# Optimization experiments

Hardware: AMD Instinct MI355X
Metric: run time of the kernel (lower is better)

The kernel has to match this reference:

```python
import jax, jax.numpy as jnp
import numpy as np

N, IN, H, C = 50000, 128, 4, 32
E = 800000
NEG_SLOPE = 0.2


def setup_inputs() -> dict:
    key = jax.random.key(0)
    ks = jax.random.split(key, 8)
    x = jax.random.normal(ks[0], (N, IN), dtype=jnp.float32)
    edge_index = jax.random.randint(ks[1], (2, E), 0, N, dtype=jnp.int64)
    s = 0.1
    W = jax.random.normal(ks[2], (H * C, IN), dtype=jnp.float32) * s
    att_src = jax.random.normal(ks[3], (1, H, C), dtype=jnp.float32) * s
    att_dst = jax.random.normal(ks[4], (1, H, C), dtype=jnp.float32) * s
    bias = jnp.zeros((H * C,), dtype=jnp.float32)
    skip_W = jax.random.normal(ks[5], (H * C, IN), dtype=jnp.float32) * s
    skip_b = jnp.zeros((H * C,), dtype=jnp.float32)
    return {"x": x, "edge_index": edge_index, "W": W, "att_src": att_src,
            "att_dst": att_dst, "bias": bias, "skip_W": skip_W, "skip_b": skip_b}


def reference(x, edge_index, W, att_src, att_dst, bias, skip_W, skip_b):
    src, dst = edge_index[0], edge_index[1]
    # projected node features: [N, H, C]
    xp = (x @ W.T).reshape(N, H, C)
    # per-node attention logits: [N, H]
    a_src = jnp.sum(xp * att_src, axis=-1)
    a_dst = jnp.sum(xp * att_dst, axis=-1)
    # edge logits with LeakyReLU: [E, H]
    e = a_src[src] + a_dst[dst]
    e = jnp.where(e > 0, e, NEG_SLOPE * e)
    # segment softmax over incoming edges of each dst node
    m = jax.ops.segment_max(e, dst, num_segments=N)  # [N, H]
    ex = jnp.exp(e - m[dst])
    denom = jax.ops.segment_sum(ex, dst, num_segments=N)  # [N, H]
    alpha = ex / (denom[dst] + 1e-16)
    # weighted messages and scatter-add aggregation: [N, H, C]
    msg = alpha[:, :, None] * xp[src]
    agg = jax.ops.segment_sum(msg, dst, num_segments=N)
    x_gat = agg.reshape(N, H * C) + bias
    x_skip = x @ skip_W.T + skip_b
    return jax.nn.elu(x_gat + x_skip)
```

## Files before the change

### kernel.cpp

```cpp
#include <hip/hip_runtime.h>
#include <hip/hip_bf16.h>


#define NN 50000
#define EE 800000
#define FD 128
#define NEG_SLOPE 0.2f

#define SCB 1024
#define NB_SC ((NN + SCB - 1) / SCB)
#define NB_HIST (EE / 256)
#define NB_CONVW 32
#define NB_MFMA (NN / 16)

typedef __attribute__((ext_vector_type(8))) short short8;
typedef __attribute__((ext_vector_type(4))) float f32x4;

__device__ inline ushort f2b(float f) {
    __hip_bfloat16 h = __float2bfloat16(f);
    return *reinterpret_cast<ushort*>(&h);
}
__device__ inline float b2f(ushort u) {
    union { float f; unsigned int i; } c;
    c.i = ((unsigned int)u) << 16;
    return c.f;
}

__global__ __launch_bounds__(256) void gat_pre_kernel(
    const int* __restrict__ idx, int* __restrict__ count, int* __restrict__ rank,
    const float* __restrict__ W, const float* __restrict__ skip_W,
    ushort* __restrict__ wb)
{
    int b = blockIdx.x;
    if (b < NB_HIST) {
        int k = b * 256 + threadIdx.x;
        int d = idx[EE + k];
        rank[k] = atomicAdd(&count[d], 1);
    } else {
        int i = ((b - NB_HIST) * 256 + threadIdx.x) * 4;
        int row = i >> 7;
        int colb = i & 127;
        const float* src = (row < 128) ? (W + row * FD + colb)
                                       : (skip_W + (row - 128) * FD + colb);
        float4 v = *reinterpret_cast<const float4*>(src);
        ushort4 o;
        o.x = f2b(v.x); o.y = f2b(v.y); o.z = f2b(v.z); o.w = f2b(v.w);
        *reinterpret_cast<ushort4*>(wb + i) = o;
    }
}

__global__ __launch_bounds__(1024) void gat_blocksum_kernel(
    const int* __restrict__ count, int* __restrict__ bsum)
{
    __shared__ int ws[16];
    int tid = threadIdx.x, lane = tid & 63, wv = tid >> 6;
    int i = blockIdx.x * SCB + tid;
    int v = (i < NN) ? count[i] : 0;
    #pragma unroll
    for (int off = 32; off; off >>= 1) v += __shfl_down(v, off, 64);
    if (lane == 0) ws[wv] = v;
    __syncthreads();
    if (wv == 0) {
        int t = (lane < 16) ? ws[lane] : 0;
        #pragma unroll
        for (int off = 8; off; off >>= 1) t += __shfl_down(t, off, 64);
        if (lane == 0) bsum[blockIdx.x] = t;
    }
}

__global__ __launch_bounds__(1024) void gat_scan_kernel(
    const int* __restrict__ count, const int* __restrict__ bsum,
    int* __restrict__ rowptr)
{
    __shared__ int ws[16];
    __shared__ int boff_s;
    int tid = threadIdx.x, lane = tid & 63, wv = tid >> 6;
    int i = blockIdx.x * SCB + tid;
    int v = (i < NN) ? count[i] : 0;
    int incl = v;
    #pragma unroll
    for (int off = 1; off < 64; off <<= 1) {
        int t = __shfl_up(incl, off, 64);
        if (lane >= off) incl += t;
    }
    if (lane == 63) ws[wv] = incl;
    __syncthreads();
    if (wv == 0) {
        int t = (lane < 16) ? ws[lane] : 0;
        int winc = t;
        #pragma unroll
        for (int off = 1; off < 16; off <<= 1) {
            int u = __shfl_up(winc, off, 64);
            if (lane >= off) winc += u;
        }
        if (lane < 16) ws[lane] = winc - t;
    } else if (wv == 1) {
        int t = (lane < blockIdx.x) ? bsum[lane] : 0;
        #pragma unroll
        for (int off = 32; off; off >>= 1) t += __shfl_down(t, off, 64);
        if (lane == 0) boff_s = t;
    }
    __syncthreads();
    int excl = boff_s + ws[wv] + incl - v;
    if (i < NN) rowptr[i] = excl;
    if (blockIdx.x == 0 && tid == 0) rowptr[NN] = EE;
}

__global__ __launch_bounds__(256) void gat_mfma_fill_kernel(
    const float* __restrict__ x, const ushort* __restrict__ wb,
    const float* __restrict__ att_src, const float* __restrict__ att_dst,
    const float* __restrict__ bias, const float* __restrict__ skip_b,
    ushort* __restrict__ xpb, float* __restrict__ a_src, float* __restrict__ a_dst,
    float* __restrict__ skip,
    const int* __restrict__ idx, const int* __restrict__ rank,
    const int* __restrict__ rowptr, int* __restrict__ col)
{
    if (blockIdx.x >= NB_MFMA) {
        int k = (blockIdx.x - NB_MFMA) * 256 + threadIdx.x;
        int d = idx[EE + k];
        col[rowptr[d] + rank[k]] = idx[k];
        return;
    }

    const int tid = threadIdx.x;
    const int w = tid >> 6;
    const int l = tid & 63;
    const int lrow = l & 15;
    const int lgrp = l >> 4;
    const int m0 = blockIdx.x * 16;
    const int is_skip = w >> 1;
    const int ncb = (w & 1) * 64;

    short8 bfrag[4][4];
    const ushort* wbase = wb + (size_t)(is_skip * 128 + ncb) * FD;
    #pragma unroll
    for (int t = 0; t < 4; ++t)
        #pragma unroll
        for (int kk = 0; kk < 4; ++kk)
            bfrag[t][kk] = *reinterpret_cast<const short8*>(
                wbase + (size_t)(t * 16 + lrow) * FD + kk * 32 + lgrp * 8);

    short8 afrag[4];
    const float* xrow = x + (size_t)(m0 + lrow) * FD + lgrp * 8;
    #pragma unroll
    for (int kk = 0; kk < 4; ++kk) {
        float4 a0 = *reinterpret_cast<const float4*>(xrow + kk * 32);
        float4 a1 = *reinterpret_cast<const float4*>(xrow + kk * 32 + 4);
        short8 af;
        af[0] = f2b(a0.x); af[1] = f2b(a0.y); af[2] = f2b(a0.z); af[3] = f2b(a0.w);
        af[4] = f2b(a1.x); af[5] = f2b(a1.y); af[6] = f2b(a1.z); af[7] = f2b(a1.w);
        afrag[kk] = af;
    }

    f32x4 acc[4];
    #pragma unroll
    for (int t = 0; t < 4; ++t) acc[t] = (f32x4){0.f, 0.f, 0.f, 0.f};

    #pragma unroll
    for (int kk = 0; kk < 4; ++kk)
        #pragma unroll
        for (int t = 0; t < 4; ++t)
            acc[t] = __builtin_amdgcn_mfma_f32_16x16x32_bf16(
                afrag[kk], bfrag[t][kk], acc[t], 0, 0, 0);

    if (is_skip) {
        #pragma unroll
        for (int t = 0; t < 4; ++t) {
            int colt = ncb + t * 16 + lrow;
            float add = skip_b[colt] + bias[colt];
            #pragma unroll
            for (int r = 0; r < 4; ++r) {
                int row = m0 + lgrp * 4 + r;
                skip[(size_t)row * FD + colt] = acc[t][r] + add;
            }
        }
    } else {
        float as[4], ad[4];
        #pragma unroll
        for (int t = 0; t < 4; ++t) {
            int colt = ncb + t * 16 + lrow;
            as[t] = att_src[colt];
            ad[t] = att_dst[colt];
            #pragma unroll
            for (int r = 0; r < 4; ++r) {
                int row = m0 + lgrp * 4 + r;
                xpb[(size_t)row * FD + colt] = f2b(acc[t][r]);
            }
        }
        const int h0 = ncb >> 5;
        #pragma unroll
        for (int r = 0; r < 4; ++r) {
            float p0 = acc[0][r] * as[0] + acc[1][r] * as[1];
            float p1 = acc[2][r] * as[2] + acc[3][r] * as[3];
            float q0 = acc[0][r] * ad[0] + acc[1][r] * ad[1];
            float q1 = acc[2][r] * ad[2] + acc[3][r] * ad[3];
            #pragma unroll
            for (int m = 1; m < 16; m <<= 1) {
                p0 += __shfl_xor(p0, m, 64);
                p1 += __shfl_xor(p1, m, 64);
                q0 += __shfl_xor(q0, m, 64);
                q1 += __shfl_xor(q1, m, 64);
            }
            if (lrow == 0) {
                int row = m0 + lgrp * 4 + r;
                a_src[(size_t)row * 4 + h0]     = p0;
                a_src[(size_t)row * 4 + h0 + 1] = p1;
                a_dst[(size_t)row * 4 + h0]     = q0;
                a_dst[(size_t)row * 4 + h0 + 1] = q1;
            }
        }
    }
}

__global__ __launch_bounds__(256) void gat_gather_kernel(
    const int* __restrict__ rowptr, const int* __restrict__ col,
    const float* __restrict__ a_src, const float* __restrict__ a_dst,
    const ushort* __restrict__ xpb, const float* __restrict__ skip,
    float* __restrict__ out)
{
    int wid = (blockIdx.x * 256 + threadIdx.x) >> 6;
    const int d = __builtin_amdgcn_readfirstlane(wid);
    int lane = threadIdx.x & 63;
    const int h = lane >> 4;
    const int ch = lane * 2;
    const float ad = a_dst[(size_t)d * 4 + h];
    const int beg = rowptr[d], end = rowptr[d + 1];
    float2 sk = *reinterpret_cast<const float2*>(skip + (size_t)d * FD + ch);

    float accx = 0.f, accy = 0.f, asum = 0.f;
    int j = beg;
    for (; j + 4 <= end; j += 4) {
        int s0 = col[j], s1 = col[j + 1], s2 = col[j + 2], s3 = col[j + 3];
        float e0 = a_src[(size_t)s0 * 4 + h] + ad;
        float e1 = a_src[(size_t)s1 * 4 + h] + ad;
        float e2 = a_src[(size_t)s2 * 4 + h] + ad;
        float e3 = a_src[(size_t)s3 * 4 + h] + ad;
        ushort2 x0 = *reinterpret_cast<const ushort2*>(xpb + (size_t)s0 * FD + ch);
        ushort2 x1 = *reinterpret_cast<const ushort2*>(xpb + (size_t)s1 * FD + ch);
        ushort2 x2 = *reinterpret_cast<const ushort2*>(xpb + (size_t)s2 * FD + ch);
        ushort2 x3 = *reinterpret_cast<const ushort2*>(xpb + (size_t)s3 * FD + ch);
        e0 = e0 > 0.f ? e0 : NEG_SLOPE * e0;
        e1 = e1 > 0.f ? e1 : NEG_SLOPE * e1;
        e2 = e2 > 0.f ? e2 : NEG_SLOPE * e2;
        e3 = e3 > 0.f ? e3 : NEG_SLOPE * e3;
        float p0 = __expf(e0), p1 = __expf(e1), p2 = __expf(e2), p3 = __expf(e3);
        asum += (p0 + p1) + (p2 + p3);
        accx += p0 * b2f(x0.x) + p1 * b2f(x1.x) + p2 * b2f(x2.x) + p3 * b2f(x3.x);
        accy += p0 * b2f(x0.y) + p1 * b2f(x1.y) + p2 * b2f(x2.y) + p3 * b2f(x3.y);
    }
    for (; j < end; ++j) {
        int s = col[j];
        float e = a_src[(size_t)s * 4 + h] + ad;
        ushort2 xv = *reinterpret_cast<const ushort2*>(xpb + (size_t)s * FD + ch);
        e = e > 0.f ? e : NEG_SLOPE * e;
        float p = __expf(e);
        asum += p;
        accx += p * b2f(xv.x);
        accy += p * b2f(xv.y);
    }
    float inv = 1.f / (asum + 1e-16f);
    float r0 = sk.x + accx * inv;
    float r1 = sk.y + accy * inv;
    r0 = r0 > 0.f ? r0 : expm1f(r0);
    r1 = r1 > 0.f ? r1 : expm1f(r1);
    *reinterpret_cast<float2*>(out + (size_t)d * FD + ch) = make_float2(r0, r1);
}

extern "C" void kernel_launch(void* const* d_in, const int* in_sizes, int n_in,
                              void* d_out, int out_size, void* d_ws, size_t ws_size,
                              hipStream_t stream)
{
    const float* x       = (const float*)d_in[0];
    const int*   idx     = (const int*)d_in[1];
    const float* W       = (const float*)d_in[2];
    const float* att_src = (const float*)d_in[3];
    const float* att_dst = (const float*)d_in[4];
    const float* bias    = (const float*)d_in[5];
    const float* skip_W  = (const float*)d_in[6];
    const float* skip_b  = (const float*)d_in[7];
    float*       out     = (float*)d_out;

    float*  ws     = (float*)d_ws;
    float*  skip   = ws;
    float*  a_src  = ws + 6400000;
    float*  a_dst  = ws + 6600000;
    int*    count  = (int*)(ws + 6800000);
    int*    rowptr = (int*)(ws + 6852000);
    int*    col    = (int*)(ws + 6956000);
    int*    rank   = (int*)(ws + 7756000);
    int*    bsum   = (int*)(ws + 8556000);
    ushort* xpb    = (ushort*)(ws + 8600000);
    ushort* wb     = (ushort*)(ws + 11900000);

    hipMemsetAsync(count, 0, (size_t)NN * sizeof(int), stream);

    gat_pre_kernel<<<NB_HIST + NB_CONVW, 256, 0, stream>>>(idx, count, rank, W, skip_W, wb);

    gat_blocksum_kernel<<<NB_SC, SCB, 0, stream>>>(count, bsum);
    gat_scan_kernel<<<NB_SC, SCB, 0, stream>>>(count, bsum, rowptr);

    gat_mfma_fill_kernel<<<NB_MFMA + NB_HIST, 256, 0, stream>>>(
        x, wb, att_src, att_dst, bias, skip_b, xpb, a_src, a_dst, skip,
        idx, rank, rowptr, col);

    gat_gather_kernel<<<(NN * 64) / 256, 256, 0, stream>>>(
        rowptr, col, a_src, a_dst, xpb, skip, out);
}
```

Before: 135.0 us.

## Vectorize histogram and CSR fill, merge scan kernels, scalarize gather indices

The histogram and CSR fill passes now handle four edges per thread with int4 loads, cutting the block count. The separate blocksum kernel is removed: each scan block sums all preceding counts itself, which saves a launch at the cost of redundant reads. In the gather kernel the column indices go through readfirstlane so source indices live in scalar registers, making the neighbor reads scalar rather than per-lane vector loads.

```diff
diff --git a/kernel.cpp b/kernel.cpp
--- a/kernel.cpp
+++ b/kernel.cpp
@@ -9,9 +9,10 @@
 
 #define SCB 1024
 #define NB_SC ((NN + SCB - 1) / SCB)
-#define NB_HIST (EE / 256)
+#define NB_PRE 782
 #define NB_CONVW 32
 #define NB_MFMA (NN / 16)
+#define NB_FILL 782
 
 typedef __attribute__((ext_vector_type(8))) short short8;
 typedef __attribute__((ext_vector_type(4))) float f32x4;
@@ -32,12 +33,18 @@
     ushort* __restrict__ wb)
 {
     int b = blockIdx.x;
-    if (b < NB_HIST) {
-        int k = b * 256 + threadIdx.x;
-        int d = idx[EE + k];
-        rank[k] = atomicAdd(&count[d], 1);
+    if (b < NB_PRE) {
+        int base = (b * 256 + threadIdx.x) * 4;
+        if (base >= EE) return;
+        int4 dd = *reinterpret_cast<const int4*>(idx + EE + base);
+        int4 rr;
+        rr.x = atomicAdd(&count[dd.x], 1);
+        rr.y = atomicAdd(&count[dd.y], 1);
+        rr.z = atomicAdd(&count[dd.z], 1);
+        rr.w = atomicAdd(&count[dd.w], 1);
+        *reinterpret_cast<int4*>(rank + base) = rr;
     } else {
-        int i = ((b - NB_HIST) * 256 + threadIdx.x) * 4;
+        int i = ((b - NB_PRE) * 256 + threadIdx.x) * 4;
         int row = i >> 7;
         int colb = i & 127;
         const float* src = (row < 128) ? (W + row * FD + colb)
@@ -49,32 +56,27 @@
     }
 }
 
-__global__ __launch_bounds__(1024) void gat_blocksum_kernel(
-    const int* __restrict__ count, int* __restrict__ bsum)
+__global__ __launch_bounds__(1024) void gat_scan_kernel(
+    const int* __restrict__ count, int* __restrict__ rowptr)
 {
     __shared__ int ws[16];
+    __shared__ int boff_s;
     int tid = threadIdx.x, lane = tid & 63, wv = tid >> 6;
-    int i = blockIdx.x * SCB + tid;
-    int v = (i < NN) ? count[i] : 0;
-    #pragma unroll
-    for (int off = 32; off; off >>= 1) v += __shfl_down(v, off, 64);
-    if (lane == 0) ws[wv] = v;
+
+    int ps = 0;
+    for (int i = tid; i < blockIdx.x * SCB; i += SCB) ps += count[i];
+    #pragma unroll
+    for (int off = 32; off; off >>= 1) ps += __shfl_down(ps, off, 64);
+    if (lane == 0) ws[wv] = ps;
     __syncthreads();
     if (wv == 0) {
         int t = (lane < 16) ? ws[lane] : 0;
         #pragma unroll
         for (int off = 8; off; off >>= 1) t += __shfl_down(t, off, 64);
-        if (lane == 0) bsum[blockIdx.x] = t;
-    }
-}
-
-__global__ __launch_bounds__(1024) void gat_scan_kernel(
-    const int* __restrict__ count, const int* __restrict__ bsum,
-    int* __restrict__ rowptr)
-{
-    __shared__ int ws[16];
-    __shared__ int boff_s;
-    int tid = threadIdx.x, lane = tid & 63, wv = tid >> 6;
+        if (lane == 0) boff_s = t;
+    }
+    __syncthreads();
+
     int i = blockIdx.x * SCB + tid;
     int v = (i < NN) ? count[i] : 0;
     int incl = v;
@@ -94,11 +96,6 @@
             if (lane >= off) winc += u;
         }
         if (lane < 16) ws[lane] = winc - t;
-    } else if (wv == 1) {
-        int t = (lane < blockIdx.x) ? bsum[lane] : 0;
-        #pragma unroll
-        for (int off = 32; off; off >>= 1) t += __shfl_down(t, off, 64);
-        if (lane == 0) boff_s = t;
     }
     __syncthreads();
     int excl = boff_s + ws[wv] + incl - v;
@@ -116,18 +113,29 @@
     const int* __restrict__ rowptr, int* __restrict__ col)
 {
     if (blockIdx.x >= NB_MFMA) {
-        int k = (blockIdx.x - NB_MFMA) * 256 + threadIdx.x;
-        int d = idx[EE + k];
-        col[rowptr[d] + rank[k]] = idx[k];
+        int base = ((blockIdx.x - NB_MFMA) * 256 + threadIdx.x) * 4;
+        if (base + 4 > EE) return;
+        int4 dd = *reinterpret_cast<const int4*>(idx + EE + base);
+        int4 rr = *reinterpret_cast<const int4*>(rank + base);
+        int4 ss = *reinterpret_cast<const int4*>(idx + base);
+        int p0 = rowptr[dd.x] + rr.x;
+        int p1 = rowptr[dd.y] + rr.y;
+        int p2 = rowptr[dd.z] + rr.z;
+        int p3 = rowptr[dd.w] + rr.w;
+        col[p0] = ss.x;
+        col[p1] = ss.y;
+        col[p2] = ss.z;
+        col[p3] = ss.w;
         return;
     }
 
+    const int p = blockIdx.x;
     const int tid = threadIdx.x;
     const int w = tid >> 6;
     const int l = tid & 63;
     const int lrow = l & 15;
     const int lgrp = l >> 4;
-    const int m0 = blockIdx.x * 16;
+    const int m0 = p * 16;
     const int is_skip = w >> 1;
     const int ncb = (w & 1) * 64;
 
@@ -230,7 +238,10 @@
     float accx = 0.f, accy = 0.f, asum = 0.f;
     int j = beg;
     for (; j + 4 <= end; j += 4) {
-        int s0 = col[j], s1 = col[j + 1], s2 = col[j + 2], s3 = col[j + 3];
+        int s0 = __builtin_amdgcn_readfirstlane(col[j]);
+        int s1 = __builtin_amdgcn_readfirstlane(col[j + 1]);
+        int s2 = __builtin_amdgcn_readfirstlane(col[j + 2]);
+        int s3 = __builtin_amdgcn_readfirstlane(col[j + 3]);
         float e0 = a_src[(size_t)s0 * 4 + h] + ad;
         float e1 = a_src[(size_t)s1 * 4 + h] + ad;
         float e2 = a_src[(size_t)s2 * 4 + h] + ad;
@@ -249,14 +260,14 @@
         accy += p0 * b2f(x0.y) + p1 * b2f(x1.y) + p2 * b2f(x2.y) + p3 * b2f(x3.y);
     }
     for (; j < end; ++j) {
-        int s = col[j];
+        int s = __builtin_amdgcn_readfirstlane(col[j]);
         float e = a_src[(size_t)s * 4 + h] + ad;
         ushort2 xv = *reinterpret_cast<const ushort2*>(xpb + (size_t)s * FD + ch);
         e = e > 0.f ? e : NEG_SLOPE * e;
-        float p = __expf(e);
-        asum += p;
-        accx += p * b2f(xv.x);
-        accy += p * b2f(xv.y);
+        float pe = __expf(e);
+        asum += pe;
+        accx += pe * b2f(xv.x);
+        accy += pe * b2f(xv.y);
     }
     float inv = 1.f / (asum + 1e-16f);
     float r0 = sk.x + accx * inv;
@@ -288,18 +299,16 @@
     int*    rowptr = (int*)(ws + 6852000);
     int*    col    = (int*)(ws + 6956000);
     int*    rank   = (int*)(ws + 7756000);
-    int*    bsum   = (int*)(ws + 8556000);
     ushort* xpb    = (ushort*)(ws + 8600000);
     ushort* wb     = (ushort*)(ws + 11900000);
 
     hipMemsetAsync(count, 0, (size_t)NN * sizeof(int), stream);
 
-    gat_pre_kernel<<<NB_HIST + NB_CONVW, 256, 0, stream>>>(idx, count, rank, W, skip_W, wb);
-
-    gat_blocksum_kernel<<<NB_SC, SCB, 0, stream>>>(count, bsum);
-    gat_scan_kernel<<<NB_SC, SCB, 0, stream>>>(count, bsum, rowptr);
-
-    gat_mfma_fill_kernel<<<NB_MFMA + NB_HIST, 256, 0, stream>>>(
+    gat_pre_kernel<<<NB_PRE + NB_CONVW, 256, 0, stream>>>(idx, count, rank, W, skip_W, wb);
+
+    gat_scan_kernel<<<NB_SC, SCB, 0, stream>>>(count, rowptr);
+
+    gat_mfma_fill_kernel<<<NB_MFMA + NB_FILL, 256, 0, stream>>>(
         x, wb, att_src, att_dst, bias, skip_b, xpb, a_src, a_dst, skip,
         idx, rank, rowptr, col);
 
```

Measured after the change: 142.2 us. 5.3% more time.
